# Optimization experiments

Hardware: AMD Instinct MI355X
Metric: run time of the kernel (lower is better)

Reference implementation:

```python
import jax, jax.numpy as jnp
import numpy as np

L, H, D, DH, DFF = 6, 8, 512, 64, 2048
EPS = 1e-5


def setup_inputs() -> dict:
    key = jax.random.key(0)
    ks = jax.random.split(key, 20)
    B, S, T = 16, 512, 512
    s = 0.02
    inp = {
        "x": jax.random.normal(ks[0], (B, S, D), jnp.float32),
        "y": jax.random.normal(ks[1], (B, T, D), jnp.float32),
        # self-attention per-head projections, stacked over layers and heads
        "Wq1": jax.random.normal(ks[2], (L, H, D, DH), jnp.float32) * s,
        "Wk1": jax.random.normal(ks[3], (L, H, D, DH), jnp.float32) * s,
        "Wv1": jax.random.normal(ks[4], (L, H, D, DH), jnp.float32) * s,
        "Wo1": jax.random.normal(ks[5], (L, D, D), jnp.float32) * s,
        # cross-attention
        "Wq2": jax.random.normal(ks[6], (L, H, D, DH), jnp.float32) * s,
        "Wk2": jax.random.normal(ks[7], (L, H, D, DH), jnp.float32) * s,
        "Wv2": jax.random.normal(ks[8], (L, H, D, DH), jnp.float32) * s,
        "Wo2": jax.random.normal(ks[9], (L, D, D), jnp.float32) * s,
        # position-wise FFN
        "W1": jax.random.normal(ks[10], (L, D, DFF), jnp.float32) * s,
        "bf1": jnp.zeros((L, DFF), jnp.float32),
        "W2": jax.random.normal(ks[11], (L, DFF, D), jnp.float32) * s,
        "bf2": jnp.zeros((L, D), jnp.float32),
        # layer norms
        "ln1_g": jnp.ones((L, D), jnp.float32), "ln1_b": jnp.zeros((L, D), jnp.float32),
        "ln2_g": jnp.ones((L, D), jnp.float32), "ln2_b": jnp.zeros((L, D), jnp.float32),
        "ln3_g": jnp.ones((L, D), jnp.float32), "ln3_b": jnp.zeros((L, D), jnp.float32),
    }
    return inp


def _layer_norm(x, g, b):
    m = jnp.mean(x, axis=-1, keepdims=True)
    v = jnp.mean(jnp.square(x - m), axis=-1, keepdims=True)
    return (x - m) * jax.lax.rsqrt(v + EPS) * g + b


def _mha(q_in, kv_in, Wq, Wk, Wv, Wo, causal):
    # Wq/Wk/Wv: [H, D, DH]; batched equivalent of the per-head Linear loop
    q = jnp.einsum("bsd,hdk->bhsk", q_in, Wq)
    k = jnp.einsum("btd,hdk->bhtk", kv_in, Wk)
    v = jnp.einsum("btd,hdk->bhtk", kv_in, Wv)
    scores = jnp.einsum("bhsk,bhtk->bhst", q, k) / jnp.sqrt(jnp.float32(DH))
    if causal:
        S, T = scores.shape[-2], scores.shape[-1]
        mask = jnp.tril(jnp.ones((S, T), bool))
        scores = jnp.where(mask, scores, -jnp.inf)
    p = jax.nn.softmax(scores, axis=-1)
    out = jnp.einsum("bhst,bhtk->bhsk", p, v)
    B, _, S, _ = out.shape
    out = out.transpose(0, 2, 1, 3).reshape(B, S, H * DH)  # concat heads (dim=2 order)
    return out @ Wo


def reference(x, y, Wq1, Wk1, Wv1, Wo1, Wq2, Wk2, Wv2, Wo2,
              W1, bf1, W2, bf2, ln1_g, ln1_b, ln2_g, ln2_b, ln3_g, ln3_b):
    for l in range(L):
        # masked self-attention + residual + LN  (dropout = identity in eval)
        a1 = _mha(x, x, Wq1[l], Wk1[l], Wv1[l], Wo1[l], causal=True)
        h1 = _layer_norm(a1 + x, ln1_g[l], ln1_b[l])
        # cross-attention (queries from decoder, K/V from encoder output y)
        a2 = _mha(h1, y, Wq2[l], Wk2[l], Wv2[l], Wo2[l], causal=False)
        h2 = _layer_norm(a2 + h1, ln2_g[l], ln2_b[l])
        # position-wise FFN (batched over all positions)
        f = jax.nn.relu(h2 @ W1[l] + bf1[l]) @ W2[l] + bf2[l]
        x = _layer_norm(f + h2, ln3_g[l], ln3_b[l])
    return x
```

## Files before the change

kernel.cpp:

```cpp
#include <hip/hip_runtime.h>

typedef __bf16 bf16;
typedef __attribute__((ext_vector_type(8))) __bf16 bf16x8;
typedef __attribute__((ext_vector_type(4))) __bf16 bf16x4;
typedef __attribute__((ext_vector_type(4))) float f32x4;

#define GL16(gp, lp) __builtin_amdgcn_global_load_lds( \
    (const __attribute__((address_space(1))) unsigned int*)(gp), \
    (__attribute__((address_space(3))) unsigned int*)(lp), 16, 0, 0)

__device__ __forceinline__ f32x4 mfma16(bf16x8 a, bf16x8 b, f32x4 c) {
  return __builtin_amdgcn_mfma_f32_16x16x32_bf16(a, b, c, 0, 0, 0);
}

template<int BN, int RELU, int BIAS, int RES, int OUTB, int VTO>
__global__ __launch_bounds__(256, (BN == 64) ? 3 : 2) void gemm_k(
    const bf16* __restrict__ A, const bf16* __restrict__ Bt,
    float* __restrict__ Cf, bf16* __restrict__ Cb,
    const float* __restrict__ bias, const bf16* __restrict__ resid,
    bf16* __restrict__ vt, int vtc0,
    int M, int N, int K)
{
  constexpr int MI = 4;
  constexpr int NI = BN / 32;
  __shared__ __align__(16) bf16 Al[2][128 * 64];
  __shared__ __align__(16) bf16 Bl[2][BN * 64];
  const int tid = threadIdx.x;
  const int wid = tid >> 6, lane = tid & 63;
  const int g = lane >> 4, l16 = lane & 15;

  int lin = blockIdx.x + gridDim.x * blockIdx.y;
  const int nwg = gridDim.x * gridDim.y;
  if ((nwg & 7) == 0) lin = (lin & 7) * (nwg >> 3) + (lin >> 3);
  const int bx = lin % gridDim.x, by = lin / gridDim.x;

  const int bm = by * 128, bn = bx * BN;
  const int wm = (wid >> 1) * 64;
  const int wn = (wid & 1) * (BN / 2);

  const f32x4 z4 = {0.f, 0.f, 0.f, 0.f};
  f32x4 acc[MI][NI];
#pragma unroll
  for (int i = 0; i < MI; ++i)
#pragma unroll
    for (int j = 0; j < NI; ++j) acc[i][j] = z4;

  const int sr = tid >> 3;
  const int scs = ((((tid & 7) * 16) ^ ((sr & 7) << 4)) >> 1);
  const bf16* Ag = A + (size_t)(bm + sr) * K + scs;
  const bf16* Bg = Bt + (size_t)(bn + sr) * K + scs;
  const size_t kstep32 = (size_t)32 * K;

  auto stage = [&](int sel, int k0) {
#pragma unroll
    for (int sw = 0; sw < 4; ++sw)
      GL16(Ag + k0 + sw * kstep32, &Al[sel][sw * 2048 + tid * 8]);
#pragma unroll
    for (int sw = 0; sw < BN / 32; ++sw)
      GL16(Bg + k0 + sw * kstep32, &Bl[sel][sw * 2048 + tid * 8]);
  };

  const int nsteps = K >> 6;
  stage(0, 0);
  int cur = 0;
  for (int s = 0; s < nsteps; ++s) {
    __builtin_amdgcn_sched_barrier(0);
    asm volatile("s_waitcnt vmcnt(0)" ::: "memory");
    __builtin_amdgcn_s_barrier();
    __builtin_amdgcn_sched_barrier(0);
    if (s + 1 < nsteps) stage(cur ^ 1, (s + 1) * 64);
    bf16x8 af[MI][2], bfr[NI][2];
#pragma unroll
    for (int mi = 0; mi < MI; ++mi) {
      const int row = wm + mi * 16 + l16;
      const int rs = (row & 7) << 4;
#pragma unroll
      for (int kh = 0; kh < 2; ++kh)
        af[mi][kh] = *(const bf16x8*)&Al[cur][row * 64 + (((g * 16 + kh * 64) ^ rs) >> 1)];
    }
#pragma unroll
    for (int ni = 0; ni < NI; ++ni) {
      const int row = wn + ni * 16 + l16;
      const int rs = (row & 7) << 4;
#pragma unroll
      for (int kh = 0; kh < 2; ++kh)
        bfr[ni][kh] = *(const bf16x8*)&Bl[cur][row * 64 + (((g * 16 + kh * 64) ^ rs) >> 1)];
    }
#pragma unroll
    for (int kh = 0; kh < 2; ++kh)
#pragma unroll
      for (int mi = 0; mi < MI; ++mi)
#pragma unroll
        for (int ni = 0; ni < NI; ++ni)
          acc[mi][ni] = mfma16(af[mi][kh], bfr[ni][kh], acc[mi][ni]);
    cur ^= 1;
  }

  if (VTO && bn >= vtc0) {
#pragma unroll
    for (int mi = 0; mi < MI; ++mi) {
#pragma unroll
      for (int ni = 0; ni < NI; ++ni) {
        const int row0 = bm + wm + mi * 16 + g * 4;
        const int gdh = bn + wn + ni * 16 + l16 - vtc0;
        const int l = gdh >> 9, h = (gdh >> 6) & 7, dh = gdh & 63;
        const int b = row0 >> 9, t0 = row0 & 511;
        bf16x4 v4;
#pragma unroll
        for (int r = 0; r < 4; ++r) v4[r] = (bf16)acc[mi][ni][r];
        *(bf16x4*)&vt[(((size_t)l * 128 + b * 8 + h) * 64 + dh) * 512 + t0] = v4;
      }
    }
    return;
  }

#pragma unroll
  for (int mi = 0; mi < MI; ++mi) {
#pragma unroll
    for (int ni = 0; ni < NI; ++ni) {
#pragma unroll
      for (int r = 0; r < 4; ++r) {
        const int row = bm + wm + mi * 16 + g * 4 + r;
        const int col = bn + wn + ni * 16 + l16;
        float v = acc[mi][ni][r];
        if (BIAS) v += bias[col];
        const size_t idx = (size_t)row * N + col;
        if (RES)  v += (float)resid[idx];
        if (RELU) v = fmaxf(v, 0.f);
        if (OUTB) Cb[idx] = (bf16)v;
        else      Cf[idx] = v;
      }
    }
  }
}

template<int CAUSAL>
__global__ __launch_bounds__(256, 4) void attn_k(
    const bf16* __restrict__ Q, const bf16* __restrict__ Kg,
    const bf16* __restrict__ VT, bf16* __restrict__ O, int qs, int kvs)
{
  __shared__ __align__(16) bf16 Kl[2][64 * 64];
  __shared__ __align__(16) bf16 Vl[2][64 * 64];
  __shared__ __align__(16) bf16 plb[4 * 16 * 64];
  const int tid = threadIdx.x;
  const int wid = tid >> 6, lane = tid & 63;
  const int g = lane >> 4, l16 = lane & 15;

  int lin = blockIdx.x + 8 * blockIdx.y + 64 * blockIdx.z;
  lin = (lin & 7) * 128 + (lin >> 3);
  const int qt = lin & 7, h = (lin >> 3) & 7, b = lin >> 6;

  const int q0 = qt * 64 + wid * 16;
  const size_t tokQ = (size_t)b * 512 + q0;

  const bf16* qp = Q + (tokQ + l16) * (size_t)qs + h * 64 + g * 8;
  const bf16x8 qf0 = *(const bf16x8*)qp;
  const bf16x8 qf1 = *(const bf16x8*)(qp + 32);

  const int sr = tid >> 3;
  const int cs2 = ((((tid & 7) * 16) ^ ((sr & 7) << 4)) >> 1);
  const bf16* Ksrc = Kg + ((size_t)b * 512 + sr) * kvs + h * 64 + cs2;
  const bf16* Vsrc = VT + (size_t)(b * 8 + h) * 64 * 512 + (size_t)sr * 512 + cs2;
  bf16* pw = plb + wid * 1024;

  auto stage = [&](int sel, int t0) {
    GL16(Ksrc + (size_t)t0 * kvs, &Kl[sel][tid * 8]);
    GL16(Ksrc + (size_t)(t0 + 32) * kvs, &Kl[sel][tid * 8 + 2048]);
    GL16(Vsrc + t0, &Vl[sel][tid * 8]);
    GL16(Vsrc + 32 * 512 + t0, &Vl[sel][tid * 8 + 2048]);
  };

  const f32x4 z4 = {0.f, 0.f, 0.f, 0.f};
  float m[4], ls[4];
  f32x4 o[4];
#pragma unroll
  for (int r = 0; r < 4; ++r) { m[r] = -1e30f; ls[r] = 0.f; o[r] = z4; }

  const int sw = (l16 & 7) << 4;
  const int ktmax = CAUSAL ? qt : 7;
  stage(0, 0);
  int cur = 0;
  for (int kt = 0; kt <= ktmax; ++kt) {
    const int t0 = kt * 64;
    __builtin_amdgcn_sched_barrier(0);
    asm volatile("s_waitcnt vmcnt(0)" ::: "memory");
    __builtin_amdgcn_s_barrier();
    if (kt < ktmax) stage(cur ^ 1, t0 + 64);

    f32x4 sc[4];
#pragma unroll
    for (int jt = 0; jt < 4; ++jt) {
      const int rk = jt * 16 + l16;
      const bf16x8 kf0 = *(const bf16x8*)&Kl[cur][rk * 64 + (((g * 16) ^ sw) >> 1)];
      const bf16x8 kf1 = *(const bf16x8*)&Kl[cur][rk * 64 + (((g * 16 + 64) ^ sw) >> 1)];
      sc[jt] = mfma16(qf0, kf0, z4);
      sc[jt] = mfma16(qf1, kf1, sc[jt]);
    }
#pragma unroll
    for (int r = 0; r < 4; ++r) {
      const int q = g * 4 + r;
      const int srow = q0 + q;
      const int qs7 = (q & 7) << 4;
      float pv[4];
      float mx = -1e30f;
#pragma unroll
      for (int jt = 0; jt < 4; ++jt) {
        float v = sc[jt][r] * 0.125f;
        if (CAUSAL && (t0 + jt * 16 + l16) > srow) v = -1e30f;
        pv[jt] = v;
        mx = fmaxf(mx, v);
      }
#pragma unroll
      for (int msk = 8; msk; msk >>= 1) mx = fmaxf(mx, __shfl_xor(mx, msk));
      const float mn = fmaxf(m[r], mx);
      const float corr = __expf(m[r] - mn);
      float s = 0.f;
#pragma unroll
      for (int jt = 0; jt < 4; ++jt) {
        const float p = __expf(pv[jt] - mn);
        s += p;
        const int sb = (((jt * 16 + l16) * 2) ^ qs7) >> 1;
        pw[q * 64 + sb] = (bf16)p;
      }
#pragma unroll
      for (int msk = 8; msk; msk >>= 1) s += __shfl_xor(s, msk);
      ls[r] = ls[r] * corr + s;
      m[r] = mn;
#pragma unroll
      for (int j = 0; j < 4; ++j) o[j][r] *= corr;
    }
    asm volatile("s_waitcnt lgkmcnt(0)" ::: "memory");
    __builtin_amdgcn_sched_barrier(0);
    const bf16x8 pa0 = *(const bf16x8*)&pw[l16 * 64 + (((g * 16) ^ sw) >> 1)];
    const bf16x8 pa1 = *(const bf16x8*)&pw[l16 * 64 + (((g * 16 + 64) ^ sw) >> 1)];
#pragma unroll
    for (int j = 0; j < 4; ++j) {
      const int rv = j * 16 + l16;
      const bf16x8 vf0 = *(const bf16x8*)&Vl[cur][rv * 64 + (((g * 16) ^ sw) >> 1)];
      const bf16x8 vf1 = *(const bf16x8*)&Vl[cur][rv * 64 + (((g * 16 + 64) ^ sw) >> 1)];
      o[j] = mfma16(pa0, vf0, o[j]);
      o[j] = mfma16(pa1, vf1, o[j]);
    }
    cur ^= 1;
  }
#pragma unroll
  for (int r = 0; r < 4; ++r) {
    const float inv = 1.f / ls[r];
    bf16* op = O + (tokQ + g * 4 + r) * 512 + h * 64;
#pragma unroll
    for (int j = 0; j < 4; ++j) op[j * 16 + l16] = (bf16)(o[j][r] * inv);
  }
}

__global__ __launch_bounds__(256) void ln_k(
    const float* __restrict__ z, const float* __restrict__ gam,
    const float* __restrict__ bet, float* __restrict__ of,
    bf16* __restrict__ ob)
{
  const int wid = threadIdx.x >> 6, lane = threadIdx.x & 63;
  const int row = blockIdx.x * 4 + wid;
  const f32x4* zr = (const f32x4*)(z + (size_t)row * 512);
  const f32x4 a = zr[lane], c = zr[lane + 64];
  float s = 0.f, ss = 0.f;
#pragma unroll
  for (int e = 0; e < 4; ++e) {
    s += a[e] + c[e];
    ss += a[e] * a[e] + c[e] * c[e];
  }
#pragma unroll
  for (int msk = 32; msk; msk >>= 1) {
    s += __shfl_xor(s, msk);
    ss += __shfl_xor(ss, msk);
  }
  const float mean = s * (1.f / 512.f);
  const float var = ss * (1.f / 512.f) - mean * mean;
  const float rstd = rsqrtf(var + 1e-5f);
  const f32x4* gp = (const f32x4*)gam;
  const f32x4* bp = (const f32x4*)bet;
  const f32x4 g0 = gp[lane], g1 = gp[lane + 64];
  const f32x4 b0 = bp[lane], b1 = bp[lane + 64];
  f32x4 o0, o1;
#pragma unroll
  for (int e = 0; e < 4; ++e) {
    o0[e] = (a[e] - mean) * rstd * g0[e] + b0[e];
    o1[e] = (c[e] - mean) * rstd * g1[e] + b1[e];
  }
  if (of) {
    f32x4* ofr = (f32x4*)(of + (size_t)row * 512);
    ofr[lane] = o0;
    ofr[lane + 64] = o1;
  }
  if (ob) {
    bf16x4 c0, c1;
#pragma unroll
    for (int e = 0; e < 4; ++e) { c0[e] = (bf16)o0[e]; c1[e] = (bf16)o1[e]; }
    bf16x4* obr = (bf16x4*)(ob + (size_t)row * 512);
    obr[lane] = c0;
    obr[lane + 64] = c1;
  }
}

__global__ void transpose_cast(const float* __restrict__ src, bf16* __restrict__ dst,
                               int R, int C, int bpl, size_t lstride, size_t boff)
{
  __shared__ float t[32][33];
  const int z = blockIdx.z;
  src += (size_t)z * R * C;
  dst += (size_t)(z / bpl) * lstride + (size_t)(z % bpl) * ((size_t)R * C) + boff;
  const int c0 = blockIdx.x * 32, r0 = blockIdx.y * 32;
  const int tx = threadIdx.x, ty = threadIdx.y;
#pragma unroll
  for (int j = 0; j < 32; j += 8)
    t[ty + j][tx] = src[(size_t)(r0 + ty + j) * C + c0 + tx];
  __syncthreads();
#pragma unroll
  for (int j = 0; j < 32; j += 8)
    dst[(size_t)(c0 + ty + j) * R + r0 + tx] = (bf16)t[tx][ty + j];
}

__global__ void cast4(const float* __restrict__ s, bf16* __restrict__ d)
{
  const int i = blockIdx.x * 256 + threadIdx.x;
  const f32x4 v = ((const f32x4*)s)[i];
  bf16x4 c;
#pragma unroll
  for (int e = 0; e < 4; ++e) c[e] = (bf16)v[e];
  ((bf16x4*)d)[i] = c;
}

extern "C" void kernel_launch(void* const* d_in, const int* in_sizes, int n_in,
                              void* d_out, int out_size, void* d_ws, size_t ws_size,
                              hipStream_t stream)
{
  (void)in_sizes; (void)n_in; (void)out_size; (void)ws_size;
  const float* x   = (const float*)d_in[0];
  const float* y   = (const float*)d_in[1];
  const float* Wq1 = (const float*)d_in[2];
  const float* Wk1 = (const float*)d_in[3];
  const float* Wv1 = (const float*)d_in[4];
  const float* Wo1 = (const float*)d_in[5];
  const float* Wq2 = (const float*)d_in[6];
  const float* Wk2 = (const float*)d_in[7];
  const float* Wv2 = (const float*)d_in[8];
  const float* Wo2 = (const float*)d_in[9];
  const float* W1  = (const float*)d_in[10];
  const float* b1  = (const float*)d_in[11];
  const float* W2  = (const float*)d_in[12];
  const float* b2  = (const float*)d_in[13];
  const float* ln1g = (const float*)d_in[14];
  const float* ln1b = (const float*)d_in[15];
  const float* ln2g = (const float*)d_in[16];
  const float* ln2b = (const float*)d_in[17];
  const float* ln3g = (const float*)d_in[18];
  const float* ln3b = (const float*)d_in[19];

  char* ws = (char*)d_ws;
  size_t off = 0;
  auto alloc = [&](size_t bytes) -> void* {
    void* p = (void*)(ws + off);
    off += (bytes + 255) & ~(size_t)255;
    return p;
  };

  bf16* wqkv1t = (bf16*)alloc((size_t)6 * 1536 * 512 * 2);
  bf16* wo1t   = (bf16*)alloc((size_t)6 * 512 * 512 * 2);
  bf16* wq2t   = (bf16*)alloc((size_t)6 * 512 * 512 * 2);
  bf16* wk2t   = (bf16*)alloc((size_t)6 * 512 * 512 * 2);
  bf16* wv2t   = (bf16*)alloc((size_t)6 * 512 * 512 * 2);
  bf16* wo2t   = (bf16*)alloc((size_t)6 * 512 * 512 * 2);
  bf16* w1t    = (bf16*)alloc((size_t)6 * 512 * 2048 * 2);
  bf16* w2t    = (bf16*)alloc((size_t)6 * 2048 * 512 * 2);
  bf16* xb   = (bf16*)alloc((size_t)8192 * 512 * 2);
  bf16* yb   = (bf16*)alloc((size_t)8192 * 512 * 2);
  bf16* qkvb = (bf16*)alloc((size_t)8192 * 1536 * 2);
  bf16* qb   = (bf16*)alloc((size_t)8192 * 512 * 2);
  bf16* ab   = (bf16*)alloc((size_t)8192 * 512 * 2);
  bf16* h1b  = (bf16*)alloc((size_t)8192 * 512 * 2);
  bf16* h2b  = (bf16*)alloc((size_t)8192 * 512 * 2);
  float* zf  = (float*)alloc((size_t)8192 * 512 * 4);
  bf16* vt1  = (bf16*)alloc((size_t)8192 * 512 * 2);
  bf16* k2all  = (bf16*)alloc((size_t)8192 * 3072 * 2);
  bf16* vt2all = (bf16*)alloc((size_t)6 * 8192 * 512 * 2);
  bf16* f1b  = qkvb;

  const dim3 tb(32, 8);
  transpose_cast<<<dim3(2, 16, 48), tb, 0, stream>>>(Wq1, wqkv1t, 512, 64, 8, (size_t)1536 * 512, 0);
  transpose_cast<<<dim3(2, 16, 48), tb, 0, stream>>>(Wk1, wqkv1t, 512, 64, 8, (size_t)1536 * 512, (size_t)512 * 512);
  transpose_cast<<<dim3(2, 16, 48), tb, 0, stream>>>(Wv1, wqkv1t, 512, 64, 8, (size_t)1536 * 512, (size_t)1024 * 512);
  transpose_cast<<<dim3(16, 16, 6), tb, 0, stream>>>(Wo1, wo1t, 512, 512, 1, (size_t)512 * 512, 0);
  transpose_cast<<<dim3(2, 16, 48), tb, 0, stream>>>(Wq2, wq2t, 512, 64, 8, (size_t)512 * 512, 0);
  transpose_cast<<<dim3(2, 16, 48), tb, 0, stream>>>(Wk2, wk2t, 512, 64, 8, (size_t)512 * 512, 0);
  transpose_cast<<<dim3(2, 16, 48), tb, 0, stream>>>(Wv2, wv2t, 512, 64, 8, (size_t)512 * 512, 0);
  transpose_cast<<<dim3(16, 16, 6), tb, 0, stream>>>(Wo2, wo2t, 512, 512, 1, (size_t)512 * 512, 0);
  transpose_cast<<<dim3(64, 16, 6), tb, 0, stream>>>(W1, w1t, 512, 2048, 1, (size_t)512 * 2048, 0);
  transpose_cast<<<dim3(16, 64, 6), tb, 0, stream>>>(W2, w2t, 2048, 512, 1, (size_t)2048 * 512, 0);
  cast4<<<4096, 256, 0, stream>>>(x, xb);
  cast4<<<4096, 256, 0, stream>>>(y, yb);

  const dim3 g512s(8, 64), g1536(12, 64), gff(16, 64), g3072(24, 64);

  gemm_k<128, 0, 0, 0, 1, 0><<<g3072, 256, 0, stream>>>(yb, wk2t, nullptr, k2all,
                                                        nullptr, nullptr, nullptr, 0, 8192, 3072, 512);
  gemm_k<128, 0, 0, 0, 1, 1><<<g3072, 256, 0, stream>>>(yb, wv2t, nullptr, nullptr,
                                                        nullptr, nullptr, vt2all, 0, 8192, 3072, 512);

  const bf16* curxb = xb;
  for (int l = 0; l < 6; ++l) {
    const bf16* WQKV1 = wqkv1t + (size_t)l * 1536 * 512;
    const bf16* WO1   = wo1t   + (size_t)l * 512 * 512;
    const bf16* WQ2   = wq2t   + (size_t)l * 512 * 512;
    const bf16* WO2   = wo2t   + (size_t)l * 512 * 512;
    const bf16* W1T   = w1t    + (size_t)l * 2048 * 512;
    const bf16* W2T   = w2t    + (size_t)l * 512 * 2048;

    gemm_k<128, 0, 0, 0, 1, 1><<<g1536, 256, 0, stream>>>(curxb, WQKV1, nullptr, qkvb,
                                                          nullptr, nullptr, vt1, 1024, 8192, 1536, 512);
    attn_k<1><<<dim3(8, 8, 16), 256, 0, stream>>>(qkvb, qkvb + 512, vt1, ab, 1536, 1536);
    gemm_k<64, 0, 0, 1, 0, 0><<<g512s, 256, 0, stream>>>(ab, WO1, zf, nullptr,
                                                         nullptr, curxb, nullptr, 0, 8192, 512, 512);
    ln_k<<<2048, 256, 0, stream>>>(zf, ln1g + l * 512, ln1b + l * 512, nullptr, h1b);

    gemm_k<64, 0, 0, 0, 1, 0><<<g512s, 256, 0, stream>>>(h1b, WQ2, nullptr, qb,
                                                         nullptr, nullptr, nullptr, 0, 8192, 512, 512);
    attn_k<0><<<dim3(8, 8, 16), 256, 0, stream>>>(qb, k2all + (size_t)l * 512,
                                                  vt2all + (size_t)l * 8192 * 512, ab, 512, 3072);
    gemm_k<64, 0, 0, 1, 0, 0><<<g512s, 256, 0, stream>>>(ab, WO2, zf, nullptr,
                                                         nullptr, h1b, nullptr, 0, 8192, 512, 512);
    ln_k<<<2048, 256, 0, stream>>>(zf, ln2g + l * 512, ln2b + l * 512, nullptr, h2b);

    gemm_k<128, 1, 1, 0, 1, 0><<<gff, 256, 0, stream>>>(h2b, W1T, nullptr, f1b,
                                                        b1 + l * 2048, nullptr, nullptr, 0, 8192, 2048, 512);
    gemm_k<64, 0, 1, 1, 0, 0><<<g512s, 256, 0, stream>>>(f1b, W2T, zf, nullptr,
                                                         b2 + l * 512, h2b, nullptr, 0, 8192, 512, 2048);
    float* outf = (l == 5) ? (float*)d_out : nullptr;
    bf16* outb  = (l == 5) ? nullptr : xb;
    ln_k<<<2048, 256, 0, stream>>>(zf, ln3g + l * 512, ln3b + l * 512, outf, outb);
    curxb = xb;
  }
}
```

Before: 1.269 ms.

## Stage V-transpose epilogue through LDS and merge cross-attn K/V projection GEMMs

The V-transposed output epilogue now writes accumulators into shared memory, then emits coalesced 16-byte stores along the time dimension, replacing scattered 8-byte strided stores. The separate K2 and V2 projection GEMMs over the encoder output are merged into one 6144-wide GEMM, using a new ldc parameter so the K half still writes to a 3072-wide buffer. This reads the encoder activations once and removes a launch, at the cost of extra barriers and LDS traffic in the epilogue.

```diff
diff --git a/kernel.cpp b/kernel.cpp
--- a/kernel.cpp
+++ b/kernel.cpp
@@ -19,12 +19,13 @@
     float* __restrict__ Cf, bf16* __restrict__ Cb,
     const float* __restrict__ bias, const bf16* __restrict__ resid,
     bf16* __restrict__ vt, int vtc0,
-    int M, int N, int K)
+    int M, int N, int ldc, int K)
 {
   constexpr int MI = 4;
   constexpr int NI = BN / 32;
-  __shared__ __align__(16) bf16 Al[2][128 * 64];
-  __shared__ __align__(16) bf16 Bl[2][BN * 64];
+  __shared__ __align__(16) bf16 smem[(2 * 128 + 2 * BN) * 64];
+  bf16* Al0 = smem;
+  bf16* Bl0 = smem + 2 * 128 * 64;
   const int tid = threadIdx.x;
   const int wid = tid >> 6, lane = tid & 63;
   const int g = lane >> 4, l16 = lane & 15;
@@ -54,10 +55,10 @@
   auto stage = [&](int sel, int k0) {
 #pragma unroll
     for (int sw = 0; sw < 4; ++sw)
-      GL16(Ag + k0 + sw * kstep32, &Al[sel][sw * 2048 + tid * 8]);
+      GL16(Ag + k0 + sw * kstep32, &Al0[sel * 8192 + sw * 2048 + tid * 8]);
 #pragma unroll
     for (int sw = 0; sw < BN / 32; ++sw)
-      GL16(Bg + k0 + sw * kstep32, &Bl[sel][sw * 2048 + tid * 8]);
+      GL16(Bg + k0 + sw * kstep32, &Bl0[sel * (BN * 64) + sw * 2048 + tid * 8]);
   };
 
   const int nsteps = K >> 6;
@@ -76,7 +77,7 @@
       const int rs = (row & 7) << 4;
 #pragma unroll
       for (int kh = 0; kh < 2; ++kh)
-        af[mi][kh] = *(const bf16x8*)&Al[cur][row * 64 + (((g * 16 + kh * 64) ^ rs) >> 1)];
+        af[mi][kh] = *(const bf16x8*)&Al0[cur * 8192 + row * 64 + (((g * 16 + kh * 64) ^ rs) >> 1)];
     }
 #pragma unroll
     for (int ni = 0; ni < NI; ++ni) {
@@ -84,7 +85,7 @@
       const int rs = (row & 7) << 4;
 #pragma unroll
       for (int kh = 0; kh < 2; ++kh)
-        bfr[ni][kh] = *(const bf16x8*)&Bl[cur][row * 64 + (((g * 16 + kh * 64) ^ rs) >> 1)];
+        bfr[ni][kh] = *(const bf16x8*)&Bl0[cur * (BN * 64) + row * 64 + (((g * 16 + kh * 64) ^ rs) >> 1)];
     }
 #pragma unroll
     for (int kh = 0; kh < 2; ++kh)
@@ -97,19 +98,31 @@
   }
 
   if (VTO && bn >= vtc0) {
+    __syncthreads();
+    bf16* stg = smem;
 #pragma unroll
     for (int mi = 0; mi < MI; ++mi) {
 #pragma unroll
       for (int ni = 0; ni < NI; ++ni) {
-        const int row0 = bm + wm + mi * 16 + g * 4;
-        const int gdh = bn + wn + ni * 16 + l16 - vtc0;
-        const int l = gdh >> 9, h = (gdh >> 6) & 7, dh = gdh & 63;
-        const int b = row0 >> 9, t0 = row0 & 511;
+        const int dhl = wn + ni * 16 + l16;
+        const int t0 = wm + mi * 16 + g * 4;
         bf16x4 v4;
 #pragma unroll
         for (int r = 0; r < 4; ++r) v4[r] = (bf16)acc[mi][ni][r];
-        *(bf16x4*)&vt[(((size_t)l * 128 + b * 8 + h) * 64 + dh) * 512 + t0] = v4;
+        *(bf16x4*)&stg[dhl * 136 + t0] = v4;
       }
+    }
+    __syncthreads();
+    const int b0 = bm >> 9, tseg = bm & 511;
+#pragma unroll
+    for (int it = 0; it < BN / 16; ++it) {
+      const int flat = it * 256 + tid;
+      const int dhl = flat >> 4;
+      const int t8 = (flat & 15) * 8;
+      const int gdh = bn + dhl - vtc0;
+      const int lL = gdh >> 9, hh = (gdh >> 6) & 7, dh = gdh & 63;
+      const bf16x8 v = *(const bf16x8*)&stg[dhl * 136 + t8];
+      *(bf16x8*)&vt[(((size_t)lL * 128 + b0 * 8 + hh) * 64 + dh) * 512 + tseg + t8] = v;
     }
     return;
   }
@@ -124,7 +137,7 @@
         const int col = bn + wn + ni * 16 + l16;
         float v = acc[mi][ni][r];
         if (BIAS) v += bias[col];
-        const size_t idx = (size_t)row * N + col;
+        const size_t idx = (size_t)row * ldc + col;
         if (RES)  v += (float)resid[idx];
         if (RELU) v = fmaxf(v, 0.f);
         if (OUTB) Cb[idx] = (bf16)v;
@@ -365,8 +378,7 @@
   bf16* wqkv1t = (bf16*)alloc((size_t)6 * 1536 * 512 * 2);
   bf16* wo1t   = (bf16*)alloc((size_t)6 * 512 * 512 * 2);
   bf16* wq2t   = (bf16*)alloc((size_t)6 * 512 * 512 * 2);
-  bf16* wk2t   = (bf16*)alloc((size_t)6 * 512 * 512 * 2);
-  bf16* wv2t   = (bf16*)alloc((size_t)6 * 512 * 512 * 2);
+  bf16* wkv2t  = (bf16*)alloc((size_t)6144 * 512 * 2);
   bf16* wo2t   = (bf16*)alloc((size_t)6 * 512 * 512 * 2);
   bf16* w1t    = (bf16*)alloc((size_t)6 * 512 * 2048 * 2);
   bf16* w2t    = (bf16*)alloc((size_t)6 * 2048 * 512 * 2);
@@ -389,20 +401,19 @@
   transpose_cast<<<dim3(2, 16, 48), tb, 0, stream>>>(Wv1, wqkv1t, 512, 64, 8, (size_t)1536 * 512, (size_t)1024 * 512);
   transpose_cast<<<dim3(16, 16, 6), tb, 0, stream>>>(Wo1, wo1t, 512, 512, 1, (size_t)512 * 512, 0);
   transpose_cast<<<dim3(2, 16, 48), tb, 0, stream>>>(Wq2, wq2t, 512, 64, 8, (size_t)512 * 512, 0);
-  transpose_cast<<<dim3(2, 16, 48), tb, 0, stream>>>(Wk2, wk2t, 512, 64, 8, (size_t)512 * 512, 0);
-  transpose_cast<<<dim3(2, 16, 48), tb, 0, stream>>>(Wv2, wv2t, 512, 64, 8, (size_t)512 * 512, 0);
+  transpose_cast<<<dim3(2, 16, 48), tb, 0, stream>>>(Wk2, wkv2t, 512, 64, 8, (size_t)512 * 512, 0);
+  transpose_cast<<<dim3(2, 16, 48), tb, 0, stream>>>(Wv2, wkv2t + (size_t)3072 * 512, 512, 64, 8, (size_t)512 * 512, 0);
   transpose_cast<<<dim3(16, 16, 6), tb, 0, stream>>>(Wo2, wo2t, 512, 512, 1, (size_t)512 * 512, 0);
   transpose_cast<<<dim3(64, 16, 6), tb, 0, stream>>>(W1, w1t, 512, 2048, 1, (size_t)512 * 2048, 0);
   transpose_cast<<<dim3(16, 64, 6), tb, 0, stream>>>(W2, w2t, 2048, 512, 1, (size_t)2048 * 512, 0);
   cast4<<<4096, 256, 0, stream>>>(x, xb);
   cast4<<<4096, 256, 0, stream>>>(y, yb);
 
-  const dim3 g512s(8, 64), g1536(12, 64), gff(16, 64), g3072(24, 64);
-
-  gemm_k<128, 0, 0, 0, 1, 0><<<g3072, 256, 0, stream>>>(yb, wk2t, nullptr, k2all,
-                                                        nullptr, nullptr, nullptr, 0, 8192, 3072, 512);
-  gemm_k<128, 0, 0, 0, 1, 1><<<g3072, 256, 0, stream>>>(yb, wv2t, nullptr, nullptr,
-                                                        nullptr, nullptr, vt2all, 0, 8192, 3072, 512);
+  const dim3 g512s(8, 64), g1536(12, 64), gff(16, 64), g6144(48, 64);
+
+  gemm_k<128, 0, 0, 0, 1, 1><<<g6144, 256, 0, stream>>>(yb, wkv2t, nullptr, k2all,
+                                                        nullptr, nullptr, vt2all, 3072,
+                                                        8192, 6144, 3072, 512);
 
   const bf16* curxb = xb;
   for (int l = 0; l < 6; ++l) {
@@ -414,24 +425,30 @@
     const bf16* W2T   = w2t    + (size_t)l * 512 * 2048;
 
     gemm_k<128, 0, 0, 0, 1, 1><<<g1536, 256, 0, stream>>>(curxb, WQKV1, nullptr, qkvb,
-                                                          nullptr, nullptr, vt1, 1024, 8192, 1536, 512);
+                                                          nullptr, nullptr, vt1, 1024,
+                                                          8192, 1536, 1536, 512);
     attn_k<1><<<dim3(8, 8, 16), 256, 0, stream>>>(qkvb, qkvb + 512, vt1, ab, 1536, 1536);
     gemm_k<64, 0, 0, 1, 0, 0><<<g512s, 256, 0, stream>>>(ab, WO1, zf, nullptr,
-                                                         nullptr, curxb, nullptr, 0, 8192, 512, 512);
+                                                         nullptr, curxb, nullptr, 0,
+                                                         8192, 512, 512, 512);
     ln_k<<<2048, 256, 0, stream>>>(zf, ln1g + l * 512, ln1b + l * 512, nullptr, h1b);
 
     gemm_k<64, 0, 0, 0, 1, 0><<<g512s, 256, 0, stream>>>(h1b, WQ2, nullptr, qb,
-                                                         nullptr, nullptr, nullptr, 0, 8192, 512, 512);
+                                                         nullptr, nullptr, nullptr, 0,
+                                                         8192, 512, 512, 512);
     attn_k<0><<<dim3(8, 8, 16), 256, 0, stream>>>(qb, k2all + (size_t)l * 512,
                                                   vt2all + (size_t)l * 8192 * 512, ab, 512, 3072);
     gemm_k<64, 0, 0, 1, 0, 0><<<g512s, 256, 0, stream>>>(ab, WO2, zf, nullptr,
-                                                         nullptr, h1b, nullptr, 0, 8192, 512, 512);
+                                                         nullptr, h1b, nullptr, 0,
+                                                         8192, 512, 512, 512);
     ln_k<<<2048, 256, 0, stream>>>(zf, ln2g + l * 512, ln2b + l * 512, nullptr, h2b);
 
     gemm_k<128, 1, 1, 0, 1, 0><<<gff, 256, 0, stream>>>(h2b, W1T, nullptr, f1b,
-                                                        b1 + l * 2048, nullptr, nullptr, 0, 8192, 2048, 512);
+                                                        b1 + l * 2048, nullptr, nullptr, 0,
+                                                        8192, 2048, 2048, 512);
     gemm_k<64, 0, 1, 1, 0, 0><<<g512s, 256, 0, stream>>>(f1b, W2T, zf, nullptr,
-                                                         b2 + l * 512, h2b, nullptr, 0, 8192, 512, 2048);
+                                                         b2 + l * 512, h2b, nullptr, 0,
+                                                         8192, 512, 512, 2048);
     float* outf = (l == 5) ? (float*)d_out : nullptr;
     bf16* outb  = (l == 5) ? nullptr : xb;
     ln_k<<<2048, 256, 0, stream>>>(zf, ln3g + l * 512, ln3b + l * 512, outf, outb);
```

Measured after the change: 1.144 ms. 9.8% less time.
